# Kernel optimization log

Hardware: AMD Instinct MI355X
Metric: run time of the kernel (lower is better)

## Reference

```python
import jax, jax.numpy as jnp
import numpy as np

N = 50000          # total nodes
B = 10             # graphs in batch
NPG = N // B       # nodes per graph (equal-sized graphs)
E = 800000         # edges
IN_DIM = 128
HID = 128
NHEAD = 4
DHEAD = HID // NHEAD
T = 1000
SLOPE = 0.2        # leaky_relu negative slope
ALPHA_L = 2.0


def _ln(x, g=None, b=None, eps=1e-5):
    mu = jnp.mean(x, axis=-1, keepdims=True)
    var = jnp.var(x, axis=-1, keepdims=True)
    y = (x - mu) * jax.lax.rsqrt(var + eps)
    if g is not None:
        y = y * g + b
    return y


def _gatv2(h, src, dst, Ws, Wd, a, b):
    # DGL GATv2Conv, share_weights=False, residual=False, bias=True, activation=gelu
    fs = (h @ Ws).reshape(N, NHEAD, DHEAD)
    fd = (h @ Wd).reshape(N, NHEAD, DHEAD)
    # per-edge attention logits [E, NHEAD]
    e = jnp.sum(jax.nn.leaky_relu(fs[src] + fd[dst], SLOPE) * a, axis=-1)
    # edge softmax grouped by destination node
    m = jax.ops.segment_max(e, dst, num_segments=N)
    ee = jnp.exp(e - m[dst])
    den = jax.ops.segment_sum(ee, dst, num_segments=N)
    alpha = ee / den[dst]                                  # [E, NHEAD]
    rst = jax.ops.segment_sum(alpha[..., None] * fs[src], dst, num_segments=N)
    rst = jax.nn.gelu(rst + b.reshape(1, NHEAD, DHEAD), approximate=False)
    return rst.reshape(N, HID)


def _forward(x, noise, sab, somab, time_emb,
             Ws0, Wd0, a0, b0, g0, be0,
             Ws1, Wd1, a1, b1, g1, be1,
             Wo1, bo1, Wo2, bo2, src, dst, t):
    # sample_q: statistics-matched signed noise
    miu = jnp.mean(x, axis=0)
    std = jnp.std(x, axis=0, ddof=1)          # torch.std is unbiased
    nz = _ln(noise) * std + miu
    nz = jnp.sign(x) * jnp.abs(nz)
    s1 = jnp.repeat(sab[t], NPG)[:, None]
    s2 = jnp.repeat(somab[t], NPG)[:, None]
    x_t = s1 * x + s2 * nz
    temb = jnp.repeat(time_emb[t], NPG, axis=0)
    # Denoising_Unet
    h = jnp.concatenate([x_t, temb], axis=1)   # [N, IN_DIM+HID]
    h = _ln(_gatv2(h, src, dst, Ws0, Wd0, a0, b0), g0, be0)
    h_in = h
    h = _gatv2(h, src, dst, Ws1, Wd1, a1, b1)
    h = _ln(h + h_in, g1, be1)                 # residual (shapes match)
    out = jax.nn.relu(h @ Wo1 + bo1) @ Wo2 + bo2
    # loss_fn
    mse = jnp.mean((out - x) ** 2)
    on = out / jnp.maximum(jnp.linalg.norm(out, axis=-1, keepdims=True), 1e-12)
    xn = x / jnp.maximum(jnp.linalg.norm(x, axis=-1, keepdims=True), 1e-12)
    cos = jnp.mean((1.0 - jnp.sum(on * xn, axis=-1)) ** ALPHA_L)
    return mse + 0.1 * cos


def setup_inputs() -> dict:
    key = jax.random.key(0)
    ks = jax.random.split(key, 26)
    betas = np.linspace(1e-4, 0.02, T, dtype=np.float64)
    ab = np.cumprod(1.0 - betas)
    s = 0.02
    in0 = IN_DIM + HID
    inp = {}
    inp['x'] = jax.random.normal(ks[0], (N, IN_DIM), jnp.float32)
    inp['noise'] = jax.random.normal(ks[1], (N, IN_DIM), jnp.float32)
    inp['src'] = jax.random.randint(ks[2], (E,), 0, N, dtype=jnp.int32)
    inp['dst'] = jax.random.randint(ks[3], (E,), 0, N, dtype=jnp.int32)
    inp['t'] = jax.random.randint(ks[4], (B,), 0, T, dtype=jnp.int32)
    inp['sab'] = jnp.asarray(np.sqrt(ab), jnp.float32)
    inp['somab'] = jnp.asarray(np.sqrt(1.0 - ab), jnp.float32)
    inp['time_emb'] = jax.random.normal(ks[5], (T, HID), jnp.float32) * s
    inp['Ws0'] = jax.random.normal(ks[6], (in0, HID), jnp.float32) * s
    inp['Wd0'] = jax.random.normal(ks[7], (in0, HID), jnp.float32) * s
    inp['a0'] = jax.random.normal(ks[8], (NHEAD, DHEAD), jnp.float32) * s
    inp['b0'] = jnp.zeros((HID,), jnp.float32)
    inp['g0'] = jnp.ones((HID,), jnp.float32)
    inp['be0'] = jnp.zeros((HID,), jnp.float32)
    inp['Ws1'] = jax.random.normal(ks[9], (HID, HID), jnp.float32) * s
    inp['Wd1'] = jax.random.normal(ks[10], (HID, HID), jnp.float32) * s
    inp['a1'] = jax.random.normal(ks[11], (NHEAD, DHEAD), jnp.float32) * s
    inp['b1'] = jnp.zeros((HID,), jnp.float32)
    inp['g1'] = jnp.ones((HID,), jnp.float32)
    inp['be1'] = jnp.zeros((HID,), jnp.float32)
    inp['Wo1'] = jax.random.normal(ks[12], (HID, HID), jnp.float32) * s
    inp['bo1'] = jnp.zeros((HID,), jnp.float32)
    inp['Wo2'] = jax.random.normal(ks[13], (HID, IN_DIM), jnp.float32) * s
    inp['bo2'] = jnp.zeros((IN_DIM,), jnp.float32)
    return inp


def reference(x, noise, src, dst, t, sab, somab, time_emb,
              Ws0, Wd0, a0, b0, g0, be0,
              Ws1, Wd1, a1, b1, g1, be1,
              Wo1, bo1, Wo2, bo2):
    return _forward(x, noise, sab, somab, time_emb,
                    Ws0, Wd0, a0, b0, g0, be0,
                    Ws1, Wd1, a1, b1, g1, be1,
                    Wo1, bo1, Wo2, bo2, src, dst, t)
```

## Files before the change

### kernel.cpp

```cpp
#include <hip/hip_runtime.h>
#include <hip/hip_bf16.h>
#include <math.h>

#define NN 50000
#define EE 800000
#define NPG 5000

typedef short bf16x8 __attribute__((ext_vector_type(8)));
typedef float f32x4 __attribute__((ext_vector_type(4)));

__device__ __forceinline__ float gelu_exact(float v) {
    return 0.5f * v * (1.0f + erff(v * 0.70710678118654752440f));
}

__device__ __forceinline__ ushort f2b(float f) {
    union { float f; uint u; } v; v.f = f;
    uint r = (v.u + 0x7fffu + ((v.u >> 16) & 1)) >> 16;
    return (ushort)r;
}
__device__ __forceinline__ uint pack2(float a, float b) {
    return (uint)f2b(a) | ((uint)f2b(b) << 16);
}
__device__ __forceinline__ float blo(uint u) {
    union { uint u; float f; } v; v.u = u << 16; return v.f;
}
__device__ __forceinline__ float bhi(uint u) {
    union { uint u; float f; } v; v.u = u & 0xffff0000u; return v.f;
}

__global__ __launch_bounds__(256) void colstats_kernel(const float* __restrict__ x,
                                                       float* __restrict__ sums, int n) {
    int tid = threadIdx.x;
    int col4 = (tid & 31) * 4;
    int rowgrp = tid >> 5;
    float s0 = 0.f, s1 = 0.f, s2 = 0.f, s3 = 0.f;
    float q0 = 0.f, q1 = 0.f, q2 = 0.f, q3 = 0.f;
    for (int r = blockIdx.x * 8 + rowgrp; r < n; r += gridDim.x * 8) {
        float4 v = *(const float4*)(x + (size_t)r * 128 + col4);
        s0 += v.x; s1 += v.y; s2 += v.z; s3 += v.w;
        q0 += v.x * v.x; q1 += v.y * v.y; q2 += v.z * v.z; q3 += v.w * v.w;
    }
    s0 += __shfl_xor(s0, 32); s1 += __shfl_xor(s1, 32);
    s2 += __shfl_xor(s2, 32); s3 += __shfl_xor(s3, 32);
    q0 += __shfl_xor(q0, 32); q1 += __shfl_xor(q1, 32);
    q2 += __shfl_xor(q2, 32); q3 += __shfl_xor(q3, 32);
    __shared__ float red[4][32][8];
    int wv = tid >> 6, l = tid & 63;
    if (l < 32) {
        float* p = red[wv][l];
        p[0] = s0; p[1] = s1; p[2] = s2; p[3] = s3;
        p[4] = q0; p[5] = q1; p[6] = q2; p[7] = q3;
    }
    __syncthreads();
    if (tid < 32) {
        float a0 = 0.f, a1 = 0.f, a2 = 0.f, a3 = 0.f;
        float b0 = 0.f, b1 = 0.f, b2 = 0.f, b3 = 0.f;
#pragma unroll
        for (int w = 0; w < 4; ++w) {
            float* p = red[w][tid];
            a0 += p[0]; a1 += p[1]; a2 += p[2]; a3 += p[3];
            b0 += p[4]; b1 += p[5]; b2 += p[6]; b3 += p[7];
        }
        int c = tid * 4;
        atomicAdd(&sums[c], a0); atomicAdd(&sums[c + 1], a1);
        atomicAdd(&sums[c + 2], a2); atomicAdd(&sums[c + 3], a3);
        atomicAdd(&sums[128 + c], b0); atomicAdd(&sums[128 + c + 1], b1);
        atomicAdd(&sums[128 + c + 2], b2); atomicAdd(&sums[128 + c + 3], b3);
    }
}

__global__ void finalize_stats_kernel(float* __restrict__ stats, int n) {
    int c = threadIdx.x;
    float sum = stats[c], sumsq = stats[128 + c];
    float mu = sum / (float)n;
    float var = (sumsq - sum * sum / (float)n) / (float)(n - 1);
    stats[256 + c] = mu;
    stats[384 + c] = sqrtf(fmaxf(var, 0.f));
}

__global__ __launch_bounds__(256) void build_h_kernel(const float* __restrict__ x,
        const float* __restrict__ noise, const int* __restrict__ t,
        const float* __restrict__ sab, const float* __restrict__ somab,
        const float* __restrict__ temb, const float* __restrict__ stats,
        ushort* __restrict__ h, int n) {
    int wid = (blockIdx.x * blockDim.x + threadIdx.x) >> 6;
    int lane = threadIdx.x & 63;
    if (wid >= n) return;
    int tt = t[wid / NPG];
    float s1 = sab[tt], s2v = somab[tt];
    float2 nz = ((const float2*)noise)[(size_t)wid * 64 + lane];
    float s = nz.x + nz.y;
    float sq = nz.x * nz.x + nz.y * nz.y;
#pragma unroll
    for (int o = 1; o < 64; o <<= 1) { s += __shfl_xor(s, o); sq += __shfl_xor(sq, o); }
    float mu = s * (1.f / 128.f);
    float var = sq * (1.f / 128.f) - mu * mu;
    float r = rsqrtf(var + 1e-5f);
    int f0 = 2 * lane, f1 = f0 + 1;
    float y0 = (nz.x - mu) * r * stats[384 + f0] + stats[256 + f0];
    float y1 = (nz.y - mu) * r * stats[384 + f1] + stats[256 + f1];
    float2 xv = ((const float2*)x)[(size_t)wid * 64 + lane];
    float sg0 = (xv.x > 0.f) ? 1.f : ((xv.x < 0.f) ? -1.f : 0.f);
    float sg1 = (xv.y > 0.f) ? 1.f : ((xv.y < 0.f) ? -1.f : 0.f);
    float n0 = sg0 * fabsf(y0);
    float n1 = sg1 * fabsf(y1);
    float xt0 = s1 * xv.x + s2v * n0;
    float xt1 = s1 * xv.y + s2v * n1;
    uint* row = (uint*)(h + (size_t)wid * 256);
    row[lane] = pack2(xt0, xt1);
    float2 te = ((const float2*)(temb + (size_t)tt * 128))[lane];
    row[64 + lane] = pack2(te.x, te.y);
}

__global__ __launch_bounds__(256) void convert_weights(const float* __restrict__ Ws0,
        const float* __restrict__ Wd0, const float* __restrict__ Ws1,
        const float* __restrict__ Wd1, const float* __restrict__ Wo1,
        const float* __restrict__ Wo2, ushort* __restrict__ Wt0,
        ushort* __restrict__ Wt1, ushort* __restrict__ Wo1t, ushort* __restrict__ Wo2t) {
    int i = blockIdx.x * 256 + threadIdx.x;
    if (i < 65536) {
        int c = i >> 8, k = i & 255;
        const float* W = (c < 128) ? Ws0 : Wd0;
        Wt0[c * 256 + k] = f2b(W[k * 128 + (c & 127)]);
    } else if (i < 98304) {
        int j = i - 65536;
        int c = j >> 7, k = j & 127;
        const float* W = (c < 128) ? Ws1 : Wd1;
        Wt1[c * 128 + k] = f2b(W[k * 128 + (c & 127)]);
    } else if (i < 114688) {
        int j = i - 98304;
        int c = j >> 7, k = j & 127;
        Wo1t[c * 128 + k] = f2b(Wo1[k * 128 + c]);
    } else if (i < 131072) {
        int j = i - 114688;
        int c = j >> 7, k = j & 127;
        Wo2t[c * 128 + k] = f2b(Wo2[k * 128 + c]);
    }
}

__global__ void hist_kernel(const int* __restrict__ dst, int* __restrict__ counts, int e) {
    int i = blockIdx.x * blockDim.x + threadIdx.x;
    if (i < e) atomicAdd(&counts[dst[i]], 1);
}

__global__ __launch_bounds__(1024) void scan_reduce_kernel(const int* __restrict__ counts,
        int* __restrict__ blockSums, int n) {
    int i = blockIdx.x * 1024 + threadIdx.x;
    int v = (i < n) ? counts[i] : 0;
#pragma unroll
    for (int o = 32; o > 0; o >>= 1) v += __shfl_down(v, o);
    __shared__ int sh[16];
    int lane = threadIdx.x & 63, wv = threadIdx.x >> 6;
    if (lane == 0) sh[wv] = v;
    __syncthreads();
    if (threadIdx.x == 0) {
        int s = 0;
#pragma unroll
        for (int k = 0; k < 16; ++k) s += sh[k];
        blockSums[blockIdx.x] = s;
    }
}

__global__ __launch_bounds__(64) void scan_offsets_kernel(const int* __restrict__ blockSums,
        int* __restrict__ blockOffs, int* __restrict__ indptr, int nb, int n) {
    int tid = threadIdx.x;
    int v = (tid < nb) ? blockSums[tid] : 0;
    int incl = v;
#pragma unroll
    for (int o = 1; o < 64; o <<= 1) {
        int tv = __shfl_up(incl, o);
        if (tid >= o) incl += tv;
    }
    if (tid < nb) blockOffs[tid] = incl - v;
    if (tid == 63) indptr[n] = incl;
}

__global__ __launch_bounds__(1024) void scan_apply_kernel(const int* __restrict__ counts,
        const int* __restrict__ blockOffs, int* __restrict__ indptr,
        int* __restrict__ cursor, int n) {
    int tid = threadIdx.x;
    int i = blockIdx.x * 1024 + tid;
    int v = (i < n) ? counts[i] : 0;
    int lane = tid & 63, wv = tid >> 6;
    int incl = v;
#pragma unroll
    for (int o = 1; o < 64; o <<= 1) {
        int tv = __shfl_up(incl, o);
        if (lane >= o) incl += tv;
    }
    __shared__ int wsum[16];
    __shared__ int woff[16];
    if (lane == 63) wsum[wv] = incl;
    __syncthreads();
    if (tid == 0) {
        int s = 0;
#pragma unroll
        for (int k = 0; k < 16; ++k) { woff[k] = s; s += wsum[k]; }
    }
    __syncthreads();
    int ex = incl - v + woff[wv] + blockOffs[blockIdx.x];
    if (i < n) { indptr[i] = ex; cursor[i] = ex; }
}

__global__ void scatter_kernel(const int* __restrict__ src, const int* __restrict__ dst,
                               int* __restrict__ cursor, int* __restrict__ csr_src, int e) {
    int i = blockIdx.x * blockDim.x + threadIdx.x;
    if (i < e) {
        int p = atomicAdd(&cursor[dst[i]], 1);
        csr_src[p] = src[i];
    }
}

template<int K, int NCOL, int EPI>
__global__ __launch_bounds__(256, 2) void mfma_gemm(const ushort* __restrict__ A,
        const ushort* __restrict__ Wt, const float* __restrict__ bias,
        ushort* __restrict__ C0, ushort* __restrict__ C1,
        float* __restrict__ Cf, int M) {
    constexpr int NFRAG = NCOL / 16;
    constexpr int KSTEPS = K / 32;
    __shared__ ushort Bs[32 * NCOL];
    int tid = threadIdx.x;
    int wave = tid >> 6, lane = tid & 63;
    int l15 = lane & 15, g = lane >> 4;
    int rowBase = blockIdx.x * 64 + wave * 16;
    int r = rowBase + l15;
    int rc = min(r, M - 1);
    const ushort* Arow = A + (size_t)rc * K + g * 8;

    f32x4 acc[NFRAG] = {};

    for (int ks = 0; ks < KSTEPS; ++ks) {
#pragma unroll
        for (int i = 0; i < NCOL / 64; ++i) {
            int ch = tid + i * 256;
            int c = ch >> 2, q = ch & 3;
            float4 v = *(const float4*)(Wt + (size_t)c * K + ks * 32 + q * 8);
            int off = c * 64 + ((q * 16) ^ ((c & 7) << 4));
            *(float4*)((char*)Bs + off) = v;
        }
        __syncthreads();
        bf16x8 af = *(const bf16x8*)(Arow + ks * 32);
        int roff = l15 * 64 + ((g * 16) ^ ((l15 & 7) << 4));
#pragma unroll
        for (int n = 0; n < NFRAG; ++n) {
            bf16x8 bf = *(const bf16x8*)((const char*)Bs + n * 1024 + roff);
            acc[n] = __builtin_amdgcn_mfma_f32_16x16x32_bf16(af, bf, acc[n], 0, 0, 0);
        }
        __syncthreads();
    }

#pragma unroll
    for (int n = 0; n < NFRAG; ++n) {
        int col = n * 16 + l15;
#pragma unroll
        for (int j = 0; j < 4; ++j) {
            int row = rowBase + g * 4 + j;
            if (row < M) {
                float v = acc[n][j];
                if (EPI == 1) v = fmaxf(v + bias[col], 0.f);
                if (EPI == 2) v = v + bias[col];
                if (EPI == 2) {
                    Cf[(size_t)row * 128 + col] = v;
                } else {
                    ushort bv = f2b(v);
                    if (NCOL == 256) {
                        if (n < 8) C0[(size_t)row * 128 + col] = bv;
                        else       C1[(size_t)row * 128 + col - 128] = bv;
                    } else {
                        C0[(size_t)row * 128 + col] = bv;
                    }
                }
            }
        }
    }
}

__global__ __launch_bounds__(256) void gat_kernel(const ushort* __restrict__ fs,
        const ushort* __restrict__ fd, const float* __restrict__ a,
        const float* __restrict__ bias, const int* __restrict__ indptr,
        const int* __restrict__ csr_src, float* __restrict__ rst, int n) {
    int wid = (blockIdx.x * blockDim.x + threadIdx.x) >> 6;
    int lane = threadIdx.x & 63;
    if (wid >= n) return;
    int beg = indptr[wid], cnt = indptr[wid + 1] - beg;
    const int* ip = csr_src + beg;
    uint fdu = ((const uint*)fd)[(size_t)wid * 64 + lane];
    float fd0 = blo(fdu), fd1 = bhi(fdu);
    float a0 = a[2 * lane], a1 = a[2 * lane + 1];
    const uint* fsu = (const uint*)fs;
    float den = 0.f, acc0 = 0.f, acc1 = 0.f;
    int s0 = (0 < cnt) ? ip[0] : 0;
    int s1 = (1 < cnt) ? ip[1] : 0;
    int s2 = (2 < cnt) ? ip[2] : 0;
    int s3 = (3 < cnt) ? ip[3] : 0;
    uint v0 = fsu[(size_t)s0 * 64 + lane];
    uint v1 = fsu[(size_t)s1 * 64 + lane];
    uint v2 = fsu[(size_t)s2 * 64 + lane];
    uint v3 = fsu[(size_t)s3 * 64 + lane];
    int i0 = (4 < cnt) ? ip[4] : 0;
    int i1 = (5 < cnt) ? ip[5] : 0;
    int i2 = (6 < cnt) ? ip[6] : 0;
    int i3 = (7 < cnt) ? ip[7] : 0;
    for (int j = 0; j < cnt; ++j) {
        uint cur = v0;
        v0 = v1; v1 = v2; v2 = v3;
        v3 = fsu[(size_t)i0 * 64 + lane];
        i0 = i1; i1 = i2; i2 = i3;
        i3 = (j + 8 < cnt) ? ip[j + 8] : 0;
        float c0 = blo(cur), c1 = bhi(cur);
        float t0 = c0 + fd0; t0 = (t0 > 0.f ? t0 : 0.2f * t0) * a0;
        float t1 = c1 + fd1; t1 = (t1 > 0.f ? t1 : 0.2f * t1) * a1;
        float p = t0 + t1;
        p += __shfl_xor(p, 1); p += __shfl_xor(p, 2);
        p += __shfl_xor(p, 4); p += __shfl_xor(p, 8);
        float w = __expf(p);
        den += w;
        acc0 = fmaf(w, c0, acc0);
        acc1 = fmaf(w, c1, acc1);
    }
    float inv = (cnt > 0) ? 1.f / den : 0.f;
    float r0 = gelu_exact(acc0 * inv + bias[2 * lane]);
    float r1 = gelu_exact(acc1 * inv + bias[2 * lane + 1]);
    ((float2*)rst)[(size_t)wid * 64 + lane] = make_float2(r0, r1);
}

__global__ __launch_bounds__(256) void ln_kernel(const float* __restrict__ in,
        const float* __restrict__ res, const float* __restrict__ g,
        const float* __restrict__ be, float* __restrict__ outF,
        ushort* __restrict__ outB, int n) {
    int wid = (blockIdx.x * blockDim.x + threadIdx.x) >> 6;
    int lane = threadIdx.x & 63;
    if (wid >= n) return;
    float2 v = ((const float2*)in)[(size_t)wid * 64 + lane];
    if (res) {
        float2 rr = ((const float2*)res)[(size_t)wid * 64 + lane];
        v.x += rr.x; v.y += rr.y;
    }
    float s = v.x + v.y;
    float sq = v.x * v.x + v.y * v.y;
#pragma unroll
    for (int o = 1; o < 64; o <<= 1) { s += __shfl_xor(s, o); sq += __shfl_xor(sq, o); }
    float mu = s * (1.f / 128.f);
    float var = sq * (1.f / 128.f) - mu * mu;
    float r = rsqrtf(var + 1e-5f);
    int f0 = 2 * lane, f1 = f0 + 1;
    float o0 = (v.x - mu) * r * g[f0] + be[f0];
    float o1 = (v.y - mu) * r * g[f1] + be[f1];
    if (outF) ((float2*)outF)[(size_t)wid * 64 + lane] = make_float2(o0, o1);
    if (outB) ((uint*)outB)[(size_t)wid * 64 + lane] = pack2(o0, o1);
}

__global__ __launch_bounds__(256) void loss_partial_kernel(const float* __restrict__ out,
        const float* __restrict__ x, float* __restrict__ partials, int n) {
    __shared__ float sm[8];
    int lane = threadIdx.x & 63;
    int wv = threadIdx.x >> 6;
    int gw = blockIdx.x * 4 + wv;
    float d2 = 0.f, closs = 0.f;
    for (int row = gw; row < n; row += 4096) {
        float2 o = ((const float2*)out)[(size_t)row * 64 + lane];
        float2 xv = ((const float2*)x)[(size_t)row * 64 + lane];
        float e0 = o.x - xv.x, e1 = o.y - xv.y;
        d2 += e0 * e0 + e1 * e1;
        float oo = o.x * o.x + o.y * o.y;
        float xx = xv.x * xv.x + xv.y * xv.y;
        float ox = o.x * xv.x + o.y * xv.y;
#pragma unroll
        for (int s = 1; s < 64; s <<= 1) {
            oo += __shfl_xor(oo, s); xx += __shfl_xor(xx, s); ox += __shfl_xor(ox, s);
        }
        float no = fmaxf(sqrtf(oo), 1e-12f);
        float nx = fmaxf(sqrtf(xx), 1e-12f);
        float cs = 1.f - ox / (no * nx);
        closs += cs * cs;
    }
#pragma unroll
    for (int s = 1; s < 64; s <<= 1) d2 += __shfl_xor(d2, s);
    if (lane == 0) { sm[wv] = d2; sm[4 + wv] = closs; }
    __syncthreads();
    if (threadIdx.x == 0) {
        partials[2 * blockIdx.x] = sm[0] + sm[1] + sm[2] + sm[3];
        partials[2 * blockIdx.x + 1] = sm[4] + sm[5] + sm[6] + sm[7];
    }
}

__global__ __launch_bounds__(1024) void loss_final_kernel(const float* __restrict__ partials,
        float* __restrict__ outp, int nb, int n) {
    __shared__ double sd[32];
    int tid = threadIdx.x;
    double m = 0.0, c = 0.0;
    for (int i = tid; i < nb; i += 1024) { m += partials[2 * i]; c += partials[2 * i + 1]; }
#pragma unroll
    for (int s = 1; s < 64; s <<= 1) { m += __shfl_xor(m, s); c += __shfl_xor(c, s); }
    int wv = tid >> 6, lane = tid & 63;
    if (lane == 0) { sd[wv] = m; sd[16 + wv] = c; }
    __syncthreads();
    if (tid == 0) {
        double mt = 0.0, ct = 0.0;
        for (int i = 0; i < 16; ++i) { mt += sd[i]; ct += sd[16 + i]; }
        outp[0] = (float)(mt / ((double)n * 128.0) + 0.1 * ct / (double)n);
    }
}

extern "C" void kernel_launch(void* const* d_in, const int* in_sizes, int n_in,
                              void* d_out, int out_size, void* d_ws, size_t ws_size,
                              hipStream_t stream) {
    const int N = NN, E = EE;
    const float* x     = (const float*)d_in[0];
    const float* noise = (const float*)d_in[1];
    const int*   src   = (const int*)d_in[2];
    const int*   dst   = (const int*)d_in[3];
    const int*   t     = (const int*)d_in[4];
    const float* sab   = (const float*)d_in[5];
    const float* somab = (const float*)d_in[6];
    const float* temb  = (const float*)d_in[7];
    const float* Ws0   = (const float*)d_in[8];
    const float* Wd0   = (const float*)d_in[9];
    const float* a0    = (const float*)d_in[10];
    const float* b0    = (const float*)d_in[11];
    const float* g0    = (const float*)d_in[12];
    const float* be0   = (const float*)d_in[13];
    const float* Ws1   = (const float*)d_in[14];
    const float* Wd1   = (const float*)d_in[15];
    const float* a1    = (const float*)d_in[16];
    const float* b1    = (const float*)d_in[17];
    const float* g1    = (const float*)d_in[18];
    const float* be1   = (const float*)d_in[19];
    const float* Wo1   = (const float*)d_in[20];
    const float* bo1   = (const float*)d_in[21];
    const float* Wo2   = (const float*)d_in[22];
    const float* bo2   = (const float*)d_in[23];

    float* ws = (float*)d_ws;
    ushort* hB  = (ushort*)ws;
    ushort* Pb  = (ushort*)ws;
    float*  Q   = ws;
    ushort* fsB = (ushort*)(ws + (size_t)N * 128);
    ushort* fdB = (ushort*)(ws + (size_t)N * 192);
    float*  P   = ws + (size_t)N * 256;
    float*  outb = P;
    ushort* Qb  = fsB;
    ushort* z   = fdB;
    float* wtail = ws + (size_t)N * 384;
    ushort* Wt0  = (ushort*)wtail;
    ushort* Wt1  = (ushort*)(wtail + 32768);
    ushort* Wo1t = (ushort*)(wtail + 49152);
    ushort* Wo2t = (ushort*)(wtail + 57344);
    float* stats    = wtail + 65536;
    float* partials = stats + 512;
    int* counts  = (int*)(partials + 2048);
    int* indptr  = counts + N;
    int* cursor  = indptr + N + 1;
    int* csr_src = cursor + N;
    int* blockSums = csr_src + E;
    int* blockOffs = blockSums + 64;

    hipMemsetAsync(stats, 0, 512 * sizeof(float), stream);
    hipMemsetAsync(counts, 0, (size_t)N * sizeof(int), stream);

    colstats_kernel<<<1024, 256, 0, stream>>>(x, stats, N);
    finalize_stats_kernel<<<1, 128, 0, stream>>>(stats, N);
    build_h_kernel<<<(N + 3) / 4, 256, 0, stream>>>(x, noise, t, sab, somab, temb, stats, hB, N);
    convert_weights<<<512, 256, 0, stream>>>(Ws0, Wd0, Ws1, Wd1, Wo1, Wo2, Wt0, Wt1, Wo1t, Wo2t);

    hist_kernel<<<(E + 255) / 256, 256, 0, stream>>>(dst, counts, E);
    int nScanB = (N + 1023) / 1024;
    scan_reduce_kernel<<<nScanB, 1024, 0, stream>>>(counts, blockSums, N);
    scan_offsets_kernel<<<1, 64, 0, stream>>>(blockSums, blockOffs, indptr, nScanB, N);
    scan_apply_kernel<<<nScanB, 1024, 0, stream>>>(counts, blockOffs, indptr, cursor, N);
    scatter_kernel<<<(E + 255) / 256, 256, 0, stream>>>(src, dst, cursor, csr_src, E);

    int gemmGrid = (N + 63) / 64;
    mfma_gemm<256, 256, 0><<<gemmGrid, 256, 0, stream>>>(hB, Wt0, nullptr, fsB, fdB, nullptr, N);
    gat_kernel<<<(N + 3) / 4, 256, 0, stream>>>(fsB, fdB, a0, b0, indptr, csr_src, P, N);
    ln_kernel<<<(N + 3) / 4, 256, 0, stream>>>(P, nullptr, g0, be0, P, Pb, N);

    mfma_gemm<128, 256, 0><<<gemmGrid, 256, 0, stream>>>(Pb, Wt1, nullptr, fsB, fdB, nullptr, N);
    gat_kernel<<<(N + 3) / 4, 256, 0, stream>>>(fsB, fdB, a1, b1, indptr, csr_src, Q, N);
    ln_kernel<<<(N + 3) / 4, 256, 0, stream>>>(Q, P, g1, be1, nullptr, Qb, N);

    mfma_gemm<128, 128, 1><<<gemmGrid, 256, 0, stream>>>(Qb, Wo1t, bo1, z, nullptr, nullptr, N);
    mfma_gemm<128, 128, 2><<<gemmGrid, 256, 0, stream>>>(z, Wo2t, bo2, nullptr, nullptr, outb, N);

    loss_partial_kernel<<<1024, 256, 0, stream>>>(outb, x, partials, N);
    loss_final_kernel<<<1, 1024, 0, stream>>>(partials, (float*)d_out, 1024, N);
}
```

Baseline: 457.6 us.

## Keep full weight tile resident in LDS and fuse GAT aggregation with LayerNorm

Measured after the change: 473.7 us. 1.04x slower.

```diff
diff --git a/kernel.cpp b/kernel.cpp
--- a/kernel.cpp
+++ b/kernel.cpp
@@ -26,6 +26,10 @@
 }
 __device__ __forceinline__ float bhi(uint u) {
     union { uint u; float f; } v; v.u = u & 0xffff0000u; return v.f;
+}
+
+__global__ void probe_kernel(int* sink) {
+    if (blockIdx.x == 99999) sink[0] = 1;
 }
 
 __global__ __launch_bounds__(256) void colstats_kernel(const float* __restrict__ x,
@@ -211,74 +215,74 @@
     }
 }
 
-template<int K, int NCOL, int EPI>
-__global__ __launch_bounds__(256, 2) void mfma_gemm(const ushort* __restrict__ A,
+template<int K, int EPI>
+__global__ __launch_bounds__(256, 2) void gemm_resW(const ushort* __restrict__ A,
         const ushort* __restrict__ Wt, const float* __restrict__ bias,
-        ushort* __restrict__ C0, ushort* __restrict__ C1,
-        float* __restrict__ Cf, int M) {
-    constexpr int NFRAG = NCOL / 16;
-    constexpr int KSTEPS = K / 32;
-    __shared__ ushort Bs[32 * NCOL];
+        ushort* __restrict__ C0, float* __restrict__ Cf, int M) {
+    constexpr int K2 = K * 2;
+    __shared__ ushort Wl[128 * K];
     int tid = threadIdx.x;
     int wave = tid >> 6, lane = tid & 63;
     int l15 = lane & 15, g = lane >> 4;
-    int rowBase = blockIdx.x * 64 + wave * 16;
-    int r = rowBase + l15;
-    int rc = min(r, M - 1);
-    const ushort* Arow = A + (size_t)rc * K + g * 8;
-
-    f32x4 acc[NFRAG] = {};
-
-    for (int ks = 0; ks < KSTEPS; ++ks) {
-#pragma unroll
-        for (int i = 0; i < NCOL / 64; ++i) {
-            int ch = tid + i * 256;
-            int c = ch >> 2, q = ch & 3;
-            float4 v = *(const float4*)(Wt + (size_t)c * K + ks * 32 + q * 8);
-            int off = c * 64 + ((q * 16) ^ ((c & 7) << 4));
-            *(float4*)((char*)Bs + off) = v;
+
+#pragma unroll
+    for (int it = 0; it < K / 16; ++it) {
+        int q = (it * 256 + tid) * 16;
+        int col = q / K2, qk = q % K2;
+        int srcb = col * K2 + (qk ^ ((col & 7) << 4));
+        *(float4*)((char*)Wl + q) = *(const float4*)((const char*)Wt + srcb);
+    }
+    __syncthreads();
+
+    int rowBase = blockIdx.x * 256 + wave * 64;
+    f32x4 acc[4][8] = {};
+
+#pragma unroll
+    for (int ks = 0; ks < K / 32; ++ks) {
+        bf16x8 af[4];
+#pragma unroll
+        for (int fr = 0; fr < 4; ++fr) {
+            int row = rowBase + fr * 16 + l15;
+            int rc = min(row, M - 1);
+            af[fr] = *(const bf16x8*)(A + (size_t)rc * K + ks * 32 + g * 8);
         }
-        __syncthreads();
-        bf16x8 af = *(const bf16x8*)(Arow + ks * 32);
-        int roff = l15 * 64 + ((g * 16) ^ ((l15 & 7) << 4));
-#pragma unroll
-        for (int n = 0; n < NFRAG; ++n) {
-            bf16x8 bf = *(const bf16x8*)((const char*)Bs + n * 1024 + roff);
-            acc[n] = __builtin_amdgcn_mfma_f32_16x16x32_bf16(af, bf, acc[n], 0, 0, 0);
+#pragma unroll
+        for (int n = 0; n < 8; ++n) {
+            int col = n * 16 + l15;
+            int boff = col * K2 + (((ks * 64 + g * 16)) ^ ((col & 7) << 4));
+            bf16x8 bf = *(const bf16x8*)((const char*)Wl + boff);
+#pragma unroll
+            for (int fr = 0; fr < 4; ++fr)
+                acc[fr][n] = __builtin_amdgcn_mfma_f32_16x16x32_bf16(af[fr], bf, acc[fr][n], 0, 0, 0);
         }
-        __syncthreads();
-    }
-
-#pragma unroll
-    for (int n = 0; n < NFRAG; ++n) {
-        int col = n * 16 + l15;
-#pragma unroll
-        for (int j = 0; j < 4; ++j) {
-            int row = rowBase + g * 4 + j;
-            if (row < M) {
-                float v = acc[n][j];
-                if (EPI == 1) v = fmaxf(v + bias[col], 0.f);
-                if (EPI == 2) v = v + bias[col];
-                if (EPI == 2) {
-                    Cf[(size_t)row * 128 + col] = v;
-                } else {
-                    ushort bv = f2b(v);
-                    if (NCOL == 256) {
-                        if (n < 8) C0[(size_t)row * 128 + col] = bv;
-                        else       C1[(size_t)row * 128 + col - 128] = bv;
-                    } else {
-                        C0[(size_t)row * 128 + col] = bv;
-                    }
+    }
+
+#pragma unroll
+    for (int fr = 0; fr < 4; ++fr) {
+#pragma unroll
+        for (int n = 0; n < 8; ++n) {
+            int col = n * 16 + l15;
+#pragma unroll
+            for (int j = 0; j < 4; ++j) {
+                int row = rowBase + fr * 16 + g * 4 + j;
+                if (row < M) {
+                    float v = acc[fr][n][j];
+                    if (EPI == 1) v = fmaxf(v + bias[col], 0.f);
+                    if (EPI == 2) v = v + bias[col];
+                    if (EPI == 2) Cf[(size_t)row * 128 + col] = v;
+                    else          C0[(size_t)row * 128 + col] = f2b(v);
                 }
             }
         }
     }
 }
 
-__global__ __launch_bounds__(256) void gat_kernel(const ushort* __restrict__ fs,
+__global__ __launch_bounds__(256) void gat_ln_kernel(const ushort* __restrict__ fs,
         const ushort* __restrict__ fd, const float* __restrict__ a,
         const float* __restrict__ bias, const int* __restrict__ indptr,
-        const int* __restrict__ csr_src, float* __restrict__ rst, int n) {
+        const int* __restrict__ csr_src, const float* __restrict__ resid,
+        const float* __restrict__ g, const float* __restrict__ be,
+        float* __restrict__ outF, ushort* __restrict__ outB, int n) {
     int wid = (blockIdx.x * blockDim.x + threadIdx.x) >> 6;
     int lane = threadIdx.x & 63;
     if (wid >= n) return;
@@ -321,31 +325,21 @@
     float inv = (cnt > 0) ? 1.f / den : 0.f;
     float r0 = gelu_exact(acc0 * inv + bias[2 * lane]);
     float r1 = gelu_exact(acc1 * inv + bias[2 * lane + 1]);
-    ((float2*)rst)[(size_t)wid * 64 + lane] = make_float2(r0, r1);
-}
-
-__global__ __launch_bounds__(256) void ln_kernel(const float* __restrict__ in,
-        const float* __restrict__ res, const float* __restrict__ g,
-        const float* __restrict__ be, float* __restrict__ outF,
-        ushort* __restrict__ outB, int n) {
-    int wid = (blockIdx.x * blockDim.x + threadIdx.x) >> 6;
-    int lane = threadIdx.x & 63;
-    if (wid >= n) return;
-    float2 v = ((const float2*)in)[(size_t)wid * 64 + lane];
-    if (res) {
-        float2 rr = ((const float2*)res)[(size_t)wid * 64 + lane];
-        v.x += rr.x; v.y += rr.y;
-    }
-    float s = v.x + v.y;
-    float sq = v.x * v.x + v.y * v.y;
+    if (resid) {
+        float2 rr = ((const float2*)resid)[(size_t)wid * 64 + lane];
+        r0 += rr.x; r1 += rr.y;
+    }
+    float s = r0 + r1;
+    float sq = r0 * r0 + r1 * r1;
 #pragma unroll
     for (int o = 1; o < 64; o <<= 1) { s += __shfl_xor(s, o); sq += __shfl_xor(sq, o); }
     float mu = s * (1.f / 128.f);
     float var = sq * (1.f / 128.f) - mu * mu;
-    float r = rsqrtf(var + 1e-5f);
-    int f0 = 2 * lane, f1 = f0 + 1;
-    float o0 = (v.x - mu) * r * g[f0] + be[f0];
-    float o1 = (v.y - mu) * r * g[f1] + be[f1];
+    float rstd = rsqrtf(var + 1e-5f);
+    float2 gg = ((const float2*)g)[lane];
+    float2 bb = ((const float2*)be)[lane];
+    float o0 = (r0 - mu) * rstd * gg.x + bb.x;
+    float o1 = (r1 - mu) * rstd * gg.y + bb.y;
     if (outF) ((float2*)outF)[(size_t)wid * 64 + lane] = make_float2(o0, o1);
     if (outB) ((uint*)outB)[(size_t)wid * 64 + lane] = pack2(o0, o1);
 }
@@ -434,13 +428,12 @@
     float* ws = (float*)d_ws;
     ushort* hB  = (ushort*)ws;
     ushort* Pb  = (ushort*)ws;
-    float*  Q   = ws;
     ushort* fsB = (ushort*)(ws + (size_t)N * 128);
     ushort* fdB = (ushort*)(ws + (size_t)N * 192);
     float*  P   = ws + (size_t)N * 256;
     float*  outb = P;
-    ushort* Qb  = fsB;
-    ushort* z   = fdB;
+    ushort* Qb  = fdB;
+    ushort* z   = fsB;
     float* wtail = ws + (size_t)N * 384;
     ushort* Wt0  = (ushort*)wtail;
     ushort* Wt1  = (ushort*)(wtail + 32768);
@@ -455,6 +448,8 @@
     int* blockSums = csr_src + E;
     int* blockOffs = blockSums + 64;
 
+    probe_kernel<<<256, 64, 0, stream>>>(blockSums);
+
     hipMemsetAsync(stats, 0, 512 * sizeof(float), stream);
     hipMemsetAsync(counts, 0, (size_t)N * sizeof(int), stream);
 
@@ -470,17 +465,17 @@
     scan_apply_kernel<<<nScanB, 1024, 0, stream>>>(counts, blockOffs, indptr, cursor, N);
     scatter_kernel<<<(E + 255) / 256, 256, 0, stream>>>(src, dst, cursor, csr_src, E);
 
-    int gemmGrid = (N + 63) / 64;
-    mfma_gemm<256, 256, 0><<<gemmGrid, 256, 0, stream>>>(hB, Wt0, nullptr, fsB, fdB, nullptr, N);
-    gat_kernel<<<(N + 3) / 4, 256, 0, stream>>>(fsB, fdB, a0, b0, indptr, csr_src, P, N);
-    ln_kernel<<<(N + 3) / 4, 256, 0, stream>>>(P, nullptr, g0, be0, P, Pb, N);
-
-    mfma_gemm<128, 256, 0><<<gemmGrid, 256, 0, stream>>>(Pb, Wt1, nullptr, fsB, fdB, nullptr, N);
-    gat_kernel<<<(N + 3) / 4, 256, 0, stream>>>(fsB, fdB, a1, b1, indptr, csr_src, Q, N);
-    ln_kernel<<<(N + 3) / 4, 256, 0, stream>>>(Q, P, g1, be1, nullptr, Qb, N);
-
-    mfma_gemm<128, 128, 1><<<gemmGrid, 256, 0, stream>>>(Qb, Wo1t, bo1, z, nullptr, nullptr, N);
-    mfma_gemm<128, 128, 2><<<gemmGrid, 256, 0, stream>>>(z, Wo2t, bo2, nullptr, nullptr, outb, N);
+    int gemmGrid = (N + 255) / 256;
+    gemm_resW<256, 0><<<gemmGrid, 256, 0, stream>>>(hB, Wt0, nullptr, fsB, nullptr, N);
+    gemm_resW<256, 0><<<gemmGrid, 256, 0, stream>>>(hB, Wt0 + 128 * 256, nullptr, fdB, nullptr, N);
+    gat_ln_kernel<<<(N + 3) / 4, 256, 0, stream>>>(fsB, fdB, a0, b0, indptr, csr_src,
+                                                   nullptr, g0, be0, P, Pb, N);
+    gemm_resW<128, 0><<<gemmGrid, 256, 0, stream>>>(Pb, Wt1, nullptr, fsB, nullptr, N);
+    gemm_resW<128, 0><<<gemmGrid, 256, 0, stream>>>(Pb, Wt1 + 128 * 128, nullptr, fdB, nullptr, N);
+    gat_ln_kernel<<<(N + 3) / 4, 256, 0, stream>>>(fsB, fdB, a1, b1, indptr, csr_src,
+                                                   P, g1, be1, nullptr, Qb, N);
+    gemm_resW<128, 1><<<gemmGrid, 256, 0, stream>>>(Qb, Wo1t, bo1, z, nullptr, N);
+    gemm_resW<128, 2><<<gemmGrid, 256, 0, stream>>>(z, Wo2t, bo2, nullptr, outb, N);
 
     loss_partial_kernel<<<1024, 256, 0, stream>>>(outb, x, partials, N);
     loss_final_kernel<<<1, 1024, 0, stream>>>(partials, (float*)d_out, 1024, N);
```
